# Kernel tuning notes

Measured on AMD Instinct MI355X. Metric: run time of the kernel, lower is better.

## Reference

```python
import jax, jax.numpy as jnp
import numpy as np

B, T, D_IN, H, D_OUT = 64, 512, 256, 1024, 256


def _gru_cell(x, h, Wi, Wh, bi, bh):
    # x: [B, in_dim], h: [B, H]; Wi: [3H, in_dim], Wh: [3H, H]
    gi = x @ Wi.T + bi  # [B, 3H]
    gh = h @ Wh.T + bh  # [B, 3H]
    i_r, i_z, i_n = jnp.split(gi, 3, axis=-1)
    h_r, h_z, h_n = jnp.split(gh, 3, axis=-1)
    r = jax.nn.sigmoid(i_r + h_r)
    z = jax.nn.sigmoid(i_z + h_z)
    n = jnp.tanh(i_n + r * h_n)
    return (1.0 - z) * n + z * h


def setup_inputs() -> dict:
    key = jax.random.key(0)
    ks = jax.random.split(key, 11)
    s_in = 1.0 / np.sqrt(D_IN)
    s_h = 1.0 / np.sqrt(H)
    return {
        "x": jax.random.normal(ks[0], (B, T, D_IN), jnp.float32),
        "Wi0": jax.random.normal(ks[1], (3 * H, D_IN), jnp.float32) * s_in,
        "Wh0": jax.random.normal(ks[2], (3 * H, H), jnp.float32) * s_h,
        "bi0": jax.random.normal(ks[3], (3 * H,), jnp.float32) * s_h,
        "bh0": jax.random.normal(ks[4], (3 * H,), jnp.float32) * s_h,
        "Wi1": jax.random.normal(ks[5], (3 * H, H), jnp.float32) * s_h,
        "Wh1": jax.random.normal(ks[6], (3 * H, H), jnp.float32) * s_h,
        "bi1": jax.random.normal(ks[7], (3 * H,), jnp.float32) * s_h,
        "bh1": jax.random.normal(ks[8], (3 * H,), jnp.float32) * s_h,
        "Wo": jax.random.normal(ks[9], (D_OUT, H), jnp.float32) * s_h,
        "bo": jax.random.normal(ks[10], (D_OUT,), jnp.float32) * s_h,
    }


def reference(x, Wi0, Wh0, bi0, bh0, Wi1, Wh1, bi1, bh1, Wo, bo):
    b = x.shape[0]
    h0 = jnp.zeros((b, H), x.dtype)
    h1 = jnp.zeros((b, H), x.dtype)

    def step(carry, x_t):
        h0, h1 = carry
        h0 = _gru_cell(x_t, h0, Wi0, Wh0, bi0, bh0)
        h1 = _gru_cell(h0, h1, Wi1, Wh1, bi1, bh1)
        return (h0, h1), None

    (h0, h1), _ = jax.lax.scan(step, (h0, h1), jnp.swapaxes(x, 0, 1))
    return h1 @ Wo.T + bo  # [B, D_OUT]
```

## Files before the change

kernel.cpp:

```cpp
#include <hip/hip_runtime.h>

constexpr int kB    = 64;
constexpr int kT    = 512;
constexpr int kDin  = 256;
constexpr int kH    = 1024;
constexpr int kH3   = 3072;
constexpr int kDout = 256;
constexpr int kHB   = kB * kH;

typedef float  f32x4  __attribute__((ext_vector_type(4)));
typedef __bf16 bf16x8 __attribute__((ext_vector_type(8)));
typedef unsigned u32x4 __attribute__((ext_vector_type(4)));
typedef unsigned long long u64;

__device__ __forceinline__ float b2f(unsigned short u) {
  union { float f; unsigned u32; } c; c.u32 = ((unsigned)u) << 16; return c.f;
}
__device__ __forceinline__ unsigned short f2b(float f) {
  union { float f; unsigned u32; } c; c.f = f;
  unsigned r = c.u32 + 0x7fffu + ((c.u32 >> 16) & 1u);
  return (unsigned short)(r >> 16);
}
__device__ __forceinline__ bf16x8 ld8(const unsigned short* p) {
  return *reinterpret_cast<const bf16x8*>(p);
}
__device__ __forceinline__ u64 ald(const u64* p) {
  return __hip_atomic_load(p, __ATOMIC_RELAXED, __HIP_MEMORY_SCOPE_AGENT);
}
__device__ __forceinline__ unsigned ald32(const unsigned* p) {
  return __hip_atomic_load(p, __ATOMIC_RELAXED, __HIP_MEMORY_SCOPE_AGENT);
}
__device__ __forceinline__ void ast32(unsigned* p, unsigned v) {
  __hip_atomic_store(p, v, __ATOMIC_RELAXED, __HIP_MEMORY_SCOPE_AGENT);
}
__device__ __forceinline__ float sigm_(float x) { return 1.f / (1.f + __expf(-x)); }
__device__ __forceinline__ float tanh_(float x) {
  return 1.f - 2.f / (__expf(2.f * x) + 1.f);
}

#define MFMA16(a, b, c) __builtin_amdgcn_mfma_f32_16x16x32_bf16((a), (b), (c), 0, 0, 0)

__global__ void gru_prep(const float* __restrict__ x,
                         const float* __restrict__ Wi0, const float* __restrict__ Wh0,
                         const float* __restrict__ bi0, const float* __restrict__ bh0,
                         const float* __restrict__ Wi1, const float* __restrict__ Wh1,
                         const float* __restrict__ bi1, const float* __restrict__ bh1,
                         unsigned short* __restrict__ xb,
                         unsigned short* __restrict__ wi0b, unsigned short* __restrict__ wh0b,
                         unsigned short* __restrict__ wi1b, unsigned short* __restrict__ wh1b,
                         unsigned short* __restrict__ r0, unsigned short* __restrict__ r1,
                         float* __restrict__ bias, unsigned* __restrict__ sync) {
  const int stride = gridDim.x * blockDim.x;
  const int g = blockIdx.x * blockDim.x + threadIdx.x;
  for (int i = g; i < kH3 * kDin; i += stride) wi0b[i] = f2b(Wi0[i]);
  for (int i = g; i < kH3 * kH; i += stride) {
    wh0b[i] = f2b(Wh0[i]); wi1b[i] = f2b(Wi1[i]); wh1b[i] = f2b(Wh1[i]);
  }
  for (int i = g; i < kB * kT * kDin; i += stride) xb[i] = f2b(x[i]);
  for (int i = g; i < kHB; i += stride) { r0[i] = 0; r1[i] = 0; }
  for (int i = g; i < kH; i += stride) {
    bias[0 * kH + i] = bi0[0 * kH + i] + bh0[0 * kH + i];
    bias[1 * kH + i] = bi0[1 * kH + i] + bh0[1 * kH + i];
    bias[2 * kH + i] = bi0[2 * kH + i];
    bias[3 * kH + i] = bh0[2 * kH + i];
    bias[4 * kH + i] = bi1[0 * kH + i] + bh1[0 * kH + i];
    bias[5 * kH + i] = bi1[1 * kH + i] + bh1[1 * kH + i];
    bias[6 * kH + i] = bi1[2 * kH + i];
    bias[7 * kH + i] = bh1[2 * kH + i];
  }
  for (int i = g; i < 1024; i += stride) sync[i] = 0;
}

__global__ void __launch_bounds__(256, 1) gru_main(
    const unsigned short* __restrict__ xb,
    const unsigned short* __restrict__ wi0, const unsigned short* __restrict__ wh0,
    const unsigned short* __restrict__ wi1, const unsigned short* __restrict__ wh1,
    const float* __restrict__ bias,
    unsigned short* __restrict__ r0, unsigned short* __restrict__ r1,
    unsigned* __restrict__ sync, const int rmode,
    const float* __restrict__ Wo, const float* __restrict__ bo,
    float* __restrict__ out) {
  __shared__ unsigned short hl0[16][1032];
  __shared__ unsigned short hl1[16][1032];
  __shared__ float red[2][4][64][5];
  __shared__ bf16x8 wlds[2][32][64];

  const int tid  = threadIdx.x;
  const int lane = tid & 63;
  const int wv   = tid >> 6;
  const int ln15 = lane & 15;
  const int quad = lane >> 4;

  const int xcd   = blockIdx.x & 7;
  const int rest  = blockIdx.x >> 3;
  const int jsub  = rest & 7;
  const int mtile = rest >> 3;
  const int pidx  = xcd * 8 + jsub;

  const int layer = wv >> 1;
  const int kh    = wv & 1;
  const int jrow  = xcd * 128 + jsub * 16 + ln15;
  const int jcol  = jrow;

  const unsigned short *pw_r, *pw_z, *pw_n, *pv_r, *pv_z, *pv_n;
  if (layer == 0) {
    pw_r = wh0 + (size_t)(0 * kH + jrow) * kH + kh * 512 + quad * 8;
    pw_z = wh0 + (size_t)(1 * kH + jrow) * kH + kh * 512 + quad * 8;
    pw_n = wh0 + (size_t)(2 * kH + jrow) * kH + kh * 512 + quad * 8;
    pv_r = wi0 + (size_t)(0 * kH + jrow) * kDin + kh * 128 + quad * 8;
    pv_z = wi0 + (size_t)(1 * kH + jrow) * kDin + kh * 128 + quad * 8;
    pv_n = wi0 + (size_t)(2 * kH + jrow) * kDin + kh * 128 + quad * 8;
  } else {
    pw_r = wh1 + (size_t)(0 * kH + jrow) * kH + kh * 512 + quad * 8;
    pw_z = wh1 + (size_t)(1 * kH + jrow) * kH + kh * 512 + quad * 8;
    pw_n = wh1 + (size_t)(2 * kH + jrow) * kH + kh * 512 + quad * 8;
    pv_r = wi1 + (size_t)(0 * kH + jrow) * kH + kh * 512 + quad * 8;
    pv_z = wi1 + (size_t)(1 * kH + jrow) * kH + kh * 512 + quad * 8;
    pv_n = wi1 + (size_t)(2 * kH + jrow) * kH + kh * 512 + quad * 8;
  }

  const float* bb = bias + layer * 4 * kH;
  const float b_r = bb[jcol];
  const float b_z = bb[kH + jcol];
  const float b_i = bb[2 * kH + jcol];
  const float b_h = bb[3 * kH + jcol];

  bf16x8 W[64];
  if (layer == 0) {
#pragma unroll
    for (int kk = 0; kk < 16; ++kk) {
      W[kk]      = ld8(pw_r + kk * 32);
      W[16 + kk] = ld8(pw_z + kk * 32);
      W[32 + kk] = ld8(pw_n + kk * 32);
    }
#pragma unroll
    for (int kk = 0; kk < 4; ++kk) {
      W[48 + kk] = ld8(pv_r + kk * 32);
      W[52 + kk] = ld8(pv_z + kk * 32);
      W[56 + kk] = ld8(pv_n + kk * 32);
    }
#pragma unroll
    for (int kk = 0; kk < 4; ++kk) W[60 + kk] = W[kk];
  } else {
#pragma unroll
    for (int kk = 0; kk < 16; ++kk) {
      W[kk]      = ld8(pv_r + kk * 32);
      W[16 + kk] = ld8(pv_z + kk * 32);
      W[32 + kk] = ld8(pv_n + kk * 32);
      W[48 + kk] = ld8(pw_r + kk * 32);
      wlds[kh][kk][lane]      = ld8(pw_z + kk * 32);
      wlds[kh][16 + kk][lane] = ld8(pw_n + kk * 32);
    }
  }

  const f32x4 z4 = {0.f, 0.f, 0.f, 0.f};
  unsigned* fl0 = sync + mtile * 64;
  unsigned* fl1 = sync + 256 + mtile * 64;

  for (int t = 0; t <= kT; ++t) {
    const bool l0c = (t < kT);
    const bool l1c = (t >= 1);
    const int s0r = rmode ? t : (t & 1);
    const int s0w = rmode ? (t + 1) : ((t + 1) & 1);
    const int s1r = rmode ? (t >= 1 ? t - 1 : 0) : ((t >= 1 ? t - 1 : 0) & 1);
    const int s1w = rmode ? t : (t & 1);

    bf16x8 xa[4];
    if (layer == 0 && l0c) {
      const unsigned short* xp = xb + (size_t)(mtile * 16 + ln15) * (kT * kDin) +
                                 t * kDin + kh * 128 + quad * 8;
#pragma unroll
      for (int i = 0; i < 4; ++i) xa[i] = ld8(xp + i * 32);
    }

    if (wv == 0) {
      for (;;) {
        int a = (int)ald32(fl0 + lane);
        int b = (int)ald32(fl1 + lane);
        if (__all(a >= t && b >= t - 1)) break;
        __builtin_amdgcn_s_sleep(8);
      }
    }
    __syncthreads();

    {
      const int r = tid >> 4, s = tid & 15;
      const unsigned short* b0 =
          r0 + (size_t)s0r * kHB + (size_t)(mtile * 16 + r) * kH + s * 64;
      const unsigned short* b1 =
          r1 + (size_t)s1r * kHB + (size_t)(mtile * 16 + r) * kH + s * 64;
      if (rmode) {
        u32x4 d0[8], d1[8];
#pragma unroll
        for (int i = 0; i < 8; ++i) d0[i] = *(const u32x4*)(b0 + i * 8);
#pragma unroll
        for (int i = 0; i < 8; ++i) d1[i] = *(const u32x4*)(b1 + i * 8);
#pragma unroll
        for (int i = 0; i < 8; ++i) *(u32x4*)&hl0[r][s * 64 + i * 8] = d0[i];
#pragma unroll
        for (int i = 0; i < 8; ++i) *(u32x4*)&hl1[r][s * 64 + i * 8] = d1[i];
      } else {
        u64 w0[16], w1[16];
#pragma unroll
        for (int i = 0; i < 16; ++i) w0[i] = ald((const u64*)b0 + i);
#pragma unroll
        for (int i = 0; i < 16; ++i) w1[i] = ald((const u64*)b1 + i);
#pragma unroll
        for (int i = 0; i < 16; ++i) *(u64*)&hl0[r][s * 64 + i * 4] = w0[i];
#pragma unroll
        for (int i = 0; i < 16; ++i) *(u64*)&hl1[r][s * 64 + i * 4] = w1[i];
      }
    }
    __syncthreads();

    f32x4 a_r = z4, a_z = z4, a_i = z4, a_h = z4;
    const bool active = (layer == 0) ? l0c : l1c;
    if (active) {
      const int kb = kh * 512;
      if (layer == 0) {
#pragma unroll
        for (int kk = 0; kk < 16; ++kk) {
          bf16x8 A = *(const bf16x8*)&hl0[ln15][kb + kk * 32 + quad * 8];
          a_r = MFMA16(A, W[kk], a_r);
          a_z = MFMA16(A, W[16 + kk], a_z);
          a_h = MFMA16(A, W[32 + kk], a_h);
        }
#pragma unroll
        for (int kk = 0; kk < 4; ++kk) {
          a_r = MFMA16(xa[kk], W[48 + kk], a_r);
          a_z = MFMA16(xa[kk], W[52 + kk], a_z);
          a_i = MFMA16(xa[kk], W[56 + kk], a_i);
        }
      } else {
#pragma unroll
        for (int kk = 0; kk < 16; ++kk) {
          bf16x8 A0 = *(const bf16x8*)&hl0[ln15][kb + kk * 32 + quad * 8];
          a_r = MFMA16(A0, W[kk], a_r);
          a_z = MFMA16(A0, W[16 + kk], a_z);
          a_i = MFMA16(A0, W[32 + kk], a_i);
          bf16x8 A1 = *(const bf16x8*)&hl1[ln15][kb + kk * 32 + quad * 8];
          a_r = MFMA16(A1, W[48 + kk], a_r);
          a_z = MFMA16(A1, wlds[kh][kk][lane], a_z);
          a_h = MFMA16(A1, wlds[kh][16 + kk][lane], a_h);
        }
      }
    }

    if (((wv == 1) && l0c) || ((wv == 3) && l1c)) {
#pragma unroll
      for (int q = 0; q < 4; ++q) {
        red[layer][0][lane][q] = a_r[q]; red[layer][1][lane][q] = a_z[q];
        red[layer][2][lane][q] = a_i[q]; red[layer][3][lane][q] = a_h[q];
      }
    }
    __syncthreads();

    if (((wv == 0) && l0c) || ((wv == 2) && l1c)) {
      float hv4[4];
#pragma unroll
      for (int q = 0; q < 4; ++q) {
        float sr = a_r[q] + red[layer][0][lane][q];
        float sz = a_z[q] + red[layer][1][lane][q];
        float si = a_i[q] + red[layer][2][lane][q];
        float sh = a_h[q] + red[layer][3][lane][q];
        float rg = sigm_(sr + b_r);
        float zg = sigm_(sz + b_z);
        float ng = tanh_(si + b_i + rg * (sh + b_h));
        float hp = (layer == 0) ? b2f(hl0[quad * 4 + q][jcol])
                                : b2f(hl1[quad * 4 + q][jcol]);
        hv4[q] = (1.f - zg) * ng + zg * hp;
      }
      unsigned short* dst = (layer == 0) ? r0 + (size_t)s0w * kHB
                                         : r1 + (size_t)s1w * kHB;
#pragma unroll
      for (int q = 0; q < 4; ++q) {
        float pv = __shfl_xor(hv4[q], 1);
        if (!(lane & 1)) {
          unsigned pk = (unsigned)f2b(hv4[q]) | ((unsigned)f2b(pv) << 16);
          unsigned* d = (unsigned*)(dst + (size_t)(mtile * 16 + quad * 4 + q) * kH +
                                    (jcol & ~1));
          ast32(d, pk);
        }
      }
    }
    __syncthreads();

    if (tid == 0 && l0c) ast32(&fl0[pidx], (unsigned)(t + 1));
    if (tid == 128 && l1c) ast32(&fl1[pidx], (unsigned)t);
  }

  if (wv == 0) {
    for (;;) {
      int f = (int)ald32(fl1 + lane);
      if (__all(f >= (int)kT)) break;
      __builtin_amdgcn_s_sleep(8);
    }
  }
  __syncthreads();
  {
    const int sfin = rmode ? kT : 0;
    const int r = tid >> 4, s = tid & 15;
    const unsigned short* b1 =
        r1 + (size_t)sfin * kHB + (size_t)(mtile * 16 + r) * kH + s * 64;
    if (rmode) {
      u32x4 d[8];
#pragma unroll
      for (int i = 0; i < 8; ++i) d[i] = *(const u32x4*)(b1 + i * 8);
#pragma unroll
      for (int i = 0; i < 8; ++i) *(u32x4*)&hl0[r][s * 64 + i * 8] = d[i];
    } else {
      u64 w[16];
#pragma unroll
      for (int i = 0; i < 16; ++i) w[i] = ald((const u64*)b1 + i);
#pragma unroll
      for (int i = 0; i < 16; ++i) *(u64*)&hl0[r][s * 64 + i * 4] = w[i];
    }
  }
  __syncthreads();
  {
    const int c  = tid & 31;
    const int rr = tid >> 5;
    const int col = jsub * 32 + c;
    const float* wr = Wo + (size_t)col * kH;
    float acc0 = bo[col], acc1 = bo[col];
#pragma unroll 8
    for (int k = 0; k < kH; k += 4) {
      float4 w4 = *reinterpret_cast<const float4*>(wr + k);
      acc0 += b2f(hl0[rr][k]) * w4.x + b2f(hl0[rr][k + 1]) * w4.y +
              b2f(hl0[rr][k + 2]) * w4.z + b2f(hl0[rr][k + 3]) * w4.w;
      acc1 += b2f(hl0[rr + 8][k]) * w4.x + b2f(hl0[rr + 8][k + 1]) * w4.y +
              b2f(hl0[rr + 8][k + 2]) * w4.z + b2f(hl0[rr + 8][k + 3]) * w4.w;
    }
    out[(mtile * 16 + rr) * kDout + col] = acc0;
    out[(mtile * 16 + rr + 8) * kDout + col] = acc1;
  }
}

extern "C" void kernel_launch(void* const* d_in, const int* in_sizes, int n_in,
                              void* d_out, int out_size, void* d_ws, size_t ws_size,
                              hipStream_t stream) {
  const float* x   = (const float*)d_in[0];
  const float* Wi0 = (const float*)d_in[1];
  const float* Wh0 = (const float*)d_in[2];
  const float* bi0 = (const float*)d_in[3];
  const float* bh0 = (const float*)d_in[4];
  const float* Wi1 = (const float*)d_in[5];
  const float* Wh1 = (const float*)d_in[6];
  const float* bi1 = (const float*)d_in[7];
  const float* bh1 = (const float*)d_in[8];
  const float* Wo  = (const float*)d_in[9];
  const float* bo  = (const float*)d_in[10];

  char* ws = (char*)d_ws;
  size_t off = 0;
  auto take = [&](size_t bytes) {
    size_t r = off;
    off += (bytes + 255) & ~(size_t)255;
    return r;
  };
  unsigned short* xb   = (unsigned short*)(ws + take((size_t)kB * kT * kDin * 2));
  unsigned short* wi0b = (unsigned short*)(ws + take((size_t)kH3 * kDin * 2));
  unsigned short* wh0b = (unsigned short*)(ws + take((size_t)kH3 * kH * 2));
  unsigned short* wi1b = (unsigned short*)(ws + take((size_t)kH3 * kH * 2));
  unsigned short* wh1b = (unsigned short*)(ws + take((size_t)kH3 * kH * 2));
  float*          bias = (float*)(ws + take(8 * kH * sizeof(float)));
  unsigned*       sync = (unsigned*)(ws + take(1024 * sizeof(unsigned)));

  const size_t slot_b = (size_t)kHB * 2;
  int rmode = 1;
  size_t ring_slots = (size_t)kT + 1;
  if (off + 2 * (ring_slots * slot_b) + (1u << 20) > ws_size) {
    rmode = 0;
    ring_slots = 2;
  }
  unsigned short* r0 = (unsigned short*)(ws + take(ring_slots * slot_b));
  unsigned short* r1 = (unsigned short*)(ws + take(ring_slots * slot_b));

  gru_prep<<<2048, 256, 0, stream>>>(x, Wi0, Wh0, bi0, bh0, Wi1, Wh1, bi1, bh1,
                                     xb, wi0b, wh0b, wi1b, wh1b, r0, r1, bias,
                                     sync);
  gru_main<<<256, 256, 0, stream>>>(xb, wi0b, wh0b, wi1b, wh1b, bias, r0, r1,
                                    sync, rmode, Wo, bo, (float*)d_out);
}
```

Measured before the change: 3.414 ms.

## Read hidden state straight from global, drop LDS staging and block barriers

Each wave now loads its MFMA A operands for the hidden states directly from the global ring buffers, using atomic loads in the relaxed mode. This removes the per-step copy into LDS and the two __syncthreads that surrounded it. The input projection MFMAs are moved ahead of the flag spin-wait so they overlap the wait. The previous hidden value stays in registers instead of being re-read from LDS. Each finishing wave publishes its progress flag with a release store instead of waiting on a final block barrier, and the spin sleep is shortened. In exchange, each wave issues more global/L2 loads per step, and correctness now depends on the release/relaxed ordering between waves.

```diff
diff --git a/kernel.cpp b/kernel.cpp
--- a/kernel.cpp
+++ b/kernel.cpp
@@ -32,6 +32,13 @@
 }
 __device__ __forceinline__ void ast32(unsigned* p, unsigned v) {
   __hip_atomic_store(p, v, __ATOMIC_RELAXED, __HIP_MEMORY_SCOPE_AGENT);
+}
+__device__ __forceinline__ bf16x8 ldA(const unsigned short* p, int rmode) {
+  if (rmode) return *reinterpret_cast<const bf16x8*>(p);
+  union { u64 d[2]; bf16x8 v; } u;
+  u.d[0] = ald((const u64*)p);
+  u.d[1] = ald((const u64*)p + 1);
+  return u.v;
 }
 __device__ __forceinline__ float sigm_(float x) { return 1.f / (1.f + __expf(-x)); }
 __device__ __forceinline__ float tanh_(float x) {
@@ -80,8 +87,6 @@
     unsigned* __restrict__ sync, const int rmode,
     const float* __restrict__ Wo, const float* __restrict__ bo,
     float* __restrict__ out) {
-  __shared__ unsigned short hl0[16][1032];
-  __shared__ unsigned short hl1[16][1032];
   __shared__ float red[2][4][64][5];
   __shared__ bf16x8 wlds[2][32][64];
 
@@ -139,8 +144,6 @@
       W[52 + kk] = ld8(pv_z + kk * 32);
       W[56 + kk] = ld8(pv_n + kk * 32);
     }
-#pragma unroll
-    for (int kk = 0; kk < 4; ++kk) W[60 + kk] = W[kk];
   } else {
 #pragma unroll
     for (int kk = 0; kk < 16; ++kk) {
@@ -157,6 +160,8 @@
   unsigned* fl0 = sync + mtile * 64;
   unsigned* fl1 = sync + 256 + mtile * 64;
 
+  float hprev[4] = {0.f, 0.f, 0.f, 0.f};
+
   for (int t = 0; t <= kT; ++t) {
     const bool l0c = (t < kT);
     const bool l1c = (t >= 1);
@@ -165,12 +170,20 @@
     const int s1r = rmode ? (t >= 1 ? t - 1 : 0) : ((t >= 1 ? t - 1 : 0) & 1);
     const int s1w = rmode ? t : (t & 1);
 
-    bf16x8 xa[4];
+    f32x4 a_r = z4, a_z = z4, a_i = z4, a_h = z4;
+
     if (layer == 0 && l0c) {
       const unsigned short* xp = xb + (size_t)(mtile * 16 + ln15) * (kT * kDin) +
                                  t * kDin + kh * 128 + quad * 8;
+      bf16x8 xa[4];
 #pragma unroll
       for (int i = 0; i < 4; ++i) xa[i] = ld8(xp + i * 32);
+#pragma unroll
+      for (int kk = 0; kk < 4; ++kk) {
+        a_r = MFMA16(xa[kk], W[48 + kk], a_r);
+        a_z = MFMA16(xa[kk], W[52 + kk], a_z);
+        a_i = MFMA16(xa[kk], W[56 + kk], a_i);
+      }
     }
 
     if (wv == 0) {
@@ -178,67 +191,34 @@
         int a = (int)ald32(fl0 + lane);
         int b = (int)ald32(fl1 + lane);
         if (__all(a >= t && b >= t - 1)) break;
-        __builtin_amdgcn_s_sleep(8);
+        __builtin_amdgcn_s_sleep(1);
       }
     }
     __syncthreads();
 
-    {
-      const int r = tid >> 4, s = tid & 15;
-      const unsigned short* b0 =
-          r0 + (size_t)s0r * kHB + (size_t)(mtile * 16 + r) * kH + s * 64;
-      const unsigned short* b1 =
-          r1 + (size_t)s1r * kHB + (size_t)(mtile * 16 + r) * kH + s * 64;
-      if (rmode) {
-        u32x4 d0[8], d1[8];
-#pragma unroll
-        for (int i = 0; i < 8; ++i) d0[i] = *(const u32x4*)(b0 + i * 8);
-#pragma unroll
-        for (int i = 0; i < 8; ++i) d1[i] = *(const u32x4*)(b1 + i * 8);
-#pragma unroll
-        for (int i = 0; i < 8; ++i) *(u32x4*)&hl0[r][s * 64 + i * 8] = d0[i];
-#pragma unroll
-        for (int i = 0; i < 8; ++i) *(u32x4*)&hl1[r][s * 64 + i * 8] = d1[i];
-      } else {
-        u64 w0[16], w1[16];
-#pragma unroll
-        for (int i = 0; i < 16; ++i) w0[i] = ald((const u64*)b0 + i);
-#pragma unroll
-        for (int i = 0; i < 16; ++i) w1[i] = ald((const u64*)b1 + i);
-#pragma unroll
-        for (int i = 0; i < 16; ++i) *(u64*)&hl0[r][s * 64 + i * 4] = w0[i];
-#pragma unroll
-        for (int i = 0; i < 16; ++i) *(u64*)&hl1[r][s * 64 + i * 4] = w1[i];
-      }
-    }
-    __syncthreads();
-
-    f32x4 a_r = z4, a_z = z4, a_i = z4, a_h = z4;
-    const bool active = (layer == 0) ? l0c : l1c;
-    if (active) {
-      const int kb = kh * 512;
-      if (layer == 0) {
+    const unsigned short* hp0 = r0 + (size_t)s0r * kHB +
+                                (size_t)(mtile * 16 + ln15) * kH + kh * 512 + quad * 8;
+    if (layer == 0) {
+      if (l0c) {
 #pragma unroll
         for (int kk = 0; kk < 16; ++kk) {
-          bf16x8 A = *(const bf16x8*)&hl0[ln15][kb + kk * 32 + quad * 8];
+          bf16x8 A = ldA(hp0 + kk * 32, rmode);
           a_r = MFMA16(A, W[kk], a_r);
           a_z = MFMA16(A, W[16 + kk], a_z);
           a_h = MFMA16(A, W[32 + kk], a_h);
         }
-#pragma unroll
-        for (int kk = 0; kk < 4; ++kk) {
-          a_r = MFMA16(xa[kk], W[48 + kk], a_r);
-          a_z = MFMA16(xa[kk], W[52 + kk], a_z);
-          a_i = MFMA16(xa[kk], W[56 + kk], a_i);
-        }
-      } else {
+      }
+    } else {
+      if (l1c) {
+        const unsigned short* hp1 = r1 + (size_t)s1r * kHB +
+                                    (size_t)(mtile * 16 + ln15) * kH + kh * 512 + quad * 8;
 #pragma unroll
         for (int kk = 0; kk < 16; ++kk) {
-          bf16x8 A0 = *(const bf16x8*)&hl0[ln15][kb + kk * 32 + quad * 8];
+          bf16x8 A0 = ldA(hp0 + kk * 32, rmode);
           a_r = MFMA16(A0, W[kk], a_r);
           a_z = MFMA16(A0, W[16 + kk], a_z);
           a_i = MFMA16(A0, W[32 + kk], a_i);
-          bf16x8 A1 = *(const bf16x8*)&hl1[ln15][kb + kk * 32 + quad * 8];
+          bf16x8 A1 = ldA(hp1 + kk * 32, rmode);
           a_r = MFMA16(A1, W[48 + kk], a_r);
           a_z = MFMA16(A1, wlds[kh][kk][lane], a_z);
           a_h = MFMA16(A1, wlds[kh][16 + kk][lane], a_h);
@@ -266,9 +246,8 @@
         float rg = sigm_(sr + b_r);
         float zg = sigm_(sz + b_z);
         float ng = tanh_(si + b_i + rg * (sh + b_h));
-        float hp = (layer == 0) ? b2f(hl0[quad * 4 + q][jcol])
-                                : b2f(hl1[quad * 4 + q][jcol]);
-        hv4[q] = (1.f - zg) * ng + zg * hp;
+        hv4[q] = (1.f - zg) * ng + zg * hprev[q];
+        hprev[q] = hv4[q];
       }
       unsigned short* dst = (layer == 0) ? r0 + (size_t)s0w * kHB
                                          : r1 + (size_t)s1w * kHB;
@@ -282,21 +261,23 @@
           ast32(d, pk);
         }
       }
-    }
-    __syncthreads();
-
-    if (tid == 0 && l0c) ast32(&fl0[pidx], (unsigned)(t + 1));
-    if (tid == 128 && l1c) ast32(&fl1[pidx], (unsigned)t);
+      if (lane == 0) {
+        unsigned* fp = (layer == 0) ? &fl0[pidx] : &fl1[pidx];
+        unsigned val = (layer == 0) ? (unsigned)(t + 1) : (unsigned)t;
+        __hip_atomic_store(fp, val, __ATOMIC_RELEASE, __HIP_MEMORY_SCOPE_AGENT);
+      }
+    }
   }
 
   if (wv == 0) {
     for (;;) {
       int f = (int)ald32(fl1 + lane);
       if (__all(f >= (int)kT)) break;
-      __builtin_amdgcn_s_sleep(8);
+      __builtin_amdgcn_s_sleep(1);
     }
   }
   __syncthreads();
+  unsigned short* hf = (unsigned short*)&wlds[0][0][0];
   {
     const int sfin = rmode ? kT : 0;
     const int r = tid >> 4, s = tid & 15;
@@ -307,13 +288,13 @@
 #pragma unroll
       for (int i = 0; i < 8; ++i) d[i] = *(const u32x4*)(b1 + i * 8);
 #pragma unroll
-      for (int i = 0; i < 8; ++i) *(u32x4*)&hl0[r][s * 64 + i * 8] = d[i];
+      for (int i = 0; i < 8; ++i) *(u32x4*)&hf[r * 1024 + s * 64 + i * 8] = d[i];
     } else {
       u64 w[16];
 #pragma unroll
       for (int i = 0; i < 16; ++i) w[i] = ald((const u64*)b1 + i);
 #pragma unroll
-      for (int i = 0; i < 16; ++i) *(u64*)&hl0[r][s * 64 + i * 4] = w[i];
+      for (int i = 0; i < 16; ++i) *(u64*)&hf[r * 1024 + s * 64 + i * 4] = w[i];
     }
   }
   __syncthreads();
@@ -326,10 +307,10 @@
 #pragma unroll 8
     for (int k = 0; k < kH; k += 4) {
       float4 w4 = *reinterpret_cast<const float4*>(wr + k);
-      acc0 += b2f(hl0[rr][k]) * w4.x + b2f(hl0[rr][k + 1]) * w4.y +
-              b2f(hl0[rr][k + 2]) * w4.z + b2f(hl0[rr][k + 3]) * w4.w;
-      acc1 += b2f(hl0[rr + 8][k]) * w4.x + b2f(hl0[rr + 8][k + 1]) * w4.y +
-              b2f(hl0[rr + 8][k + 2]) * w4.z + b2f(hl0[rr + 8][k + 3]) * w4.w;
+      acc0 += b2f(hf[rr * 1024 + k]) * w4.x + b2f(hf[rr * 1024 + k + 1]) * w4.y +
+              b2f(hf[rr * 1024 + k + 2]) * w4.z + b2f(hf[rr * 1024 + k + 3]) * w4.w;
+      acc1 += b2f(hf[(rr + 8) * 1024 + k]) * w4.x + b2f(hf[(rr + 8) * 1024 + k + 1]) * w4.y +
+              b2f(hf[(rr + 8) * 1024 + k + 2]) * w4.z + b2f(hf[(rr + 8) * 1024 + k + 3]) * w4.w;
     }
     out[(mtile * 16 + rr) * kDout + col] = acc0;
     out[(mtile * 16 + rr + 8) * kDout + col] = acc1;
```

Result: slower. 6.883 ms (+101.6%).

## Swizzle hidden-state LDS, hoist input MFMAs, keep h in registers, drop barrier

Applied to the files above, without the earlier changes.

Several changes to the persistent GRU step loop. The x-projection MFMAs move ahead of the inter-block spin-wait so they overlap with waiting. The hidden-state LDS tiles get an XOR swizzle to cut bank conflicts on MFMA operand reads. The previous hidden value is kept in fp32 registers instead of being re-read as bf16 from LDS. The trailing block barrier is replaced by the writing wave signalling its own flag after s_waitcnt, and the spin sleep is shortened. The register copy of h differs numerically from the bf16-rounded exchange copy, and dropping the barrier depends on the remaining syncthreads keeping LDS reuse ordered.

```diff
diff --git a/kernel.cpp b/kernel.cpp
--- a/kernel.cpp
+++ b/kernel.cpp
@@ -39,6 +39,10 @@
 }
 
 #define MFMA16(a, b, c) __builtin_amdgcn_mfma_f32_16x16x32_bf16((a), (b), (c), 0, 0, 0)
+
+__device__ __forceinline__ int swzcol(int C, int quad) {
+  return (C & ~63) + ((quad ^ (((C >> 3) ^ (C >> 6)) & 7)) << 3);
+}
 
 __global__ void gru_prep(const float* __restrict__ x,
                          const float* __restrict__ Wi0, const float* __restrict__ Wh0,
@@ -139,8 +143,6 @@
       W[52 + kk] = ld8(pv_z + kk * 32);
       W[56 + kk] = ld8(pv_n + kk * 32);
     }
-#pragma unroll
-    for (int kk = 0; kk < 4; ++kk) W[60 + kk] = W[kk];
   } else {
 #pragma unroll
     for (int kk = 0; kk < 16; ++kk) {
@@ -157,6 +159,8 @@
   unsigned* fl0 = sync + mtile * 64;
   unsigned* fl1 = sync + 256 + mtile * 64;
 
+  float hprev[4] = {0.f, 0.f, 0.f, 0.f};
+
   for (int t = 0; t <= kT; ++t) {
     const bool l0c = (t < kT);
     const bool l1c = (t >= 1);
@@ -165,12 +169,20 @@
     const int s1r = rmode ? (t >= 1 ? t - 1 : 0) : ((t >= 1 ? t - 1 : 0) & 1);
     const int s1w = rmode ? t : (t & 1);
 
-    bf16x8 xa[4];
+    f32x4 a_r = z4, a_z = z4, a_i = z4, a_h = z4;
+
     if (layer == 0 && l0c) {
       const unsigned short* xp = xb + (size_t)(mtile * 16 + ln15) * (kT * kDin) +
                                  t * kDin + kh * 128 + quad * 8;
+      bf16x8 xa[4];
 #pragma unroll
       for (int i = 0; i < 4; ++i) xa[i] = ld8(xp + i * 32);
+#pragma unroll
+      for (int kk = 0; kk < 4; ++kk) {
+        a_r = MFMA16(xa[kk], W[48 + kk], a_r);
+        a_z = MFMA16(xa[kk], W[52 + kk], a_z);
+        a_i = MFMA16(xa[kk], W[56 + kk], a_i);
+      }
     }
 
     if (wv == 0) {
@@ -178,7 +190,7 @@
         int a = (int)ald32(fl0 + lane);
         int b = (int)ald32(fl1 + lane);
         if (__all(a >= t && b >= t - 1)) break;
-        __builtin_amdgcn_s_sleep(8);
+        __builtin_amdgcn_s_sleep(4);
       }
     }
     __syncthreads();
@@ -196,9 +208,11 @@
 #pragma unroll
         for (int i = 0; i < 8; ++i) d1[i] = *(const u32x4*)(b1 + i * 8);
 #pragma unroll
-        for (int i = 0; i < 8; ++i) *(u32x4*)&hl0[r][s * 64 + i * 8] = d0[i];
-#pragma unroll
-        for (int i = 0; i < 8; ++i) *(u32x4*)&hl1[r][s * 64 + i * 8] = d1[i];
+        for (int i = 0; i < 8; ++i)
+          *(u32x4*)&hl0[r][s * 64 + ((i ^ s) & 7) * 8] = d0[i];
+#pragma unroll
+        for (int i = 0; i < 8; ++i)
+          *(u32x4*)&hl1[r][s * 64 + ((i ^ s) & 7) * 8] = d1[i];
       } else {
         u64 w0[16], w1[16];
 #pragma unroll
@@ -206,39 +220,34 @@
 #pragma unroll
         for (int i = 0; i < 16; ++i) w1[i] = ald((const u64*)b1 + i);
 #pragma unroll
-        for (int i = 0; i < 16; ++i) *(u64*)&hl0[r][s * 64 + i * 4] = w0[i];
-#pragma unroll
-        for (int i = 0; i < 16; ++i) *(u64*)&hl1[r][s * 64 + i * 4] = w1[i];
+        for (int i = 0; i < 16; ++i)
+          *(u64*)&hl0[r][s * 64 + (((i >> 1) ^ s) & 7) * 8 + (i & 1) * 4] = w0[i];
+#pragma unroll
+        for (int i = 0; i < 16; ++i)
+          *(u64*)&hl1[r][s * 64 + (((i >> 1) ^ s) & 7) * 8 + (i & 1) * 4] = w1[i];
       }
     }
     __syncthreads();
 
-    f32x4 a_r = z4, a_z = z4, a_i = z4, a_h = z4;
     const bool active = (layer == 0) ? l0c : l1c;
     if (active) {
       const int kb = kh * 512;
       if (layer == 0) {
 #pragma unroll
         for (int kk = 0; kk < 16; ++kk) {
-          bf16x8 A = *(const bf16x8*)&hl0[ln15][kb + kk * 32 + quad * 8];
+          bf16x8 A = *(const bf16x8*)&hl0[ln15][swzcol(kb + kk * 32, quad)];
           a_r = MFMA16(A, W[kk], a_r);
           a_z = MFMA16(A, W[16 + kk], a_z);
           a_h = MFMA16(A, W[32 + kk], a_h);
         }
-#pragma unroll
-        for (int kk = 0; kk < 4; ++kk) {
-          a_r = MFMA16(xa[kk], W[48 + kk], a_r);
-          a_z = MFMA16(xa[kk], W[52 + kk], a_z);
-          a_i = MFMA16(xa[kk], W[56 + kk], a_i);
-        }
       } else {
 #pragma unroll
         for (int kk = 0; kk < 16; ++kk) {
-          bf16x8 A0 = *(const bf16x8*)&hl0[ln15][kb + kk * 32 + quad * 8];
+          bf16x8 A0 = *(const bf16x8*)&hl0[ln15][swzcol(kb + kk * 32, quad)];
           a_r = MFMA16(A0, W[kk], a_r);
           a_z = MFMA16(A0, W[16 + kk], a_z);
           a_i = MFMA16(A0, W[32 + kk], a_i);
-          bf16x8 A1 = *(const bf16x8*)&hl1[ln15][kb + kk * 32 + quad * 8];
+          bf16x8 A1 = *(const bf16x8*)&hl1[ln15][swzcol(kb + kk * 32, quad)];
           a_r = MFMA16(A1, W[48 + kk], a_r);
           a_z = MFMA16(A1, wlds[kh][kk][lane], a_z);
           a_h = MFMA16(A1, wlds[kh][16 + kk][lane], a_h);
@@ -266,9 +275,8 @@
         float rg = sigm_(sr + b_r);
         float zg = sigm_(sz + b_z);
         float ng = tanh_(si + b_i + rg * (sh + b_h));
-        float hp = (layer == 0) ? b2f(hl0[quad * 4 + q][jcol])
-                                : b2f(hl1[quad * 4 + q][jcol]);
-        hv4[q] = (1.f - zg) * ng + zg * hp;
+        hv4[q] = (1.f - zg) * ng + zg * hprev[q];
+        hprev[q] = hv4[q];
       }
       unsigned short* dst = (layer == 0) ? r0 + (size_t)s0w * kHB
                                          : r1 + (size_t)s1w * kHB;
@@ -282,18 +290,20 @@
           ast32(d, pk);
         }
       }
-    }
-    __syncthreads();
-
-    if (tid == 0 && l0c) ast32(&fl0[pidx], (unsigned)(t + 1));
-    if (tid == 128 && l1c) ast32(&fl1[pidx], (unsigned)t);
+      asm volatile("s_waitcnt vmcnt(0)" ::: "memory");
+      if (lane == 0) {
+        unsigned* fp = (layer == 0) ? &fl0[pidx] : &fl1[pidx];
+        unsigned val = (layer == 0) ? (unsigned)(t + 1) : (unsigned)t;
+        ast32(fp, val);
+      }
+    }
   }
 
   if (wv == 0) {
     for (;;) {
       int f = (int)ald32(fl1 + lane);
       if (__all(f >= (int)kT)) break;
-      __builtin_amdgcn_s_sleep(8);
+      __builtin_amdgcn_s_sleep(4);
     }
   }
   __syncthreads();
```

After: 3.381 ms. No clear change (-1.0%).
